# Performance work log

Hardware: AMD Instinct MI355X
Metric: run time of the kernel (lower is better)

## Reference

```python
import jax, jax.numpy as jnp
from jax import lax
import numpy as np


def _gru_layer(x_seq, W_ih, W_hh, b_ih, b_hh):
    """Single GRU layer, torch gate ordering (r, z, n). x_seq: [B, T, I].
    Returns (all hidden states [B, T, H], final hidden [B, H])."""
    B, T, _ = x_seq.shape
    H = W_hh.shape[1]
    # Precompute input projections for all timesteps: [B, T, 3H]
    x_proj = jnp.einsum('bti,gi->btg', x_seq, W_ih) + b_ih

    def step(h, xp):
        hp = h @ W_hh.T + b_hh                       # [B, 3H]
        xr, xz, xn = jnp.split(xp, 3, axis=-1)
        hr, hz, hn = jnp.split(hp, 3, axis=-1)
        r = jax.nn.sigmoid(xr + hr)
        z = jax.nn.sigmoid(xz + hz)
        n = jnp.tanh(xn + r * hn)
        h_new = (1.0 - z) * n + z * h
        return h_new, h_new

    h0 = jnp.zeros((B, H), dtype=x_seq.dtype)
    hT, hs = lax.scan(step, h0, x_proj.transpose(1, 0, 2))  # scan over time
    return hs.transpose(1, 0, 2), hT


def setup_inputs() -> dict:
    key = jax.random.key(0)
    ks = jax.random.split(key, 12)
    B, T, I, H, O = 128, 1000, 64, 512, 1
    s_in = 1.0 / np.sqrt(H)  # torch GRU init scale
    d = {
        'x': jax.random.normal(ks[0], (B, T, I), jnp.float32),
        'W_ih0': jax.random.uniform(ks[1], (3 * H, I), jnp.float32, -s_in, s_in),
        'W_hh0': jax.random.uniform(ks[2], (3 * H, H), jnp.float32, -s_in, s_in),
        'b_ih0': jax.random.uniform(ks[3], (3 * H,), jnp.float32, -s_in, s_in),
        'b_hh0': jax.random.uniform(ks[4], (3 * H,), jnp.float32, -s_in, s_in),
        'W_ih1': jax.random.uniform(ks[5], (3 * H, H), jnp.float32, -s_in, s_in),
        'W_hh1': jax.random.uniform(ks[6], (3 * H, H), jnp.float32, -s_in, s_in),
        'b_ih1': jax.random.uniform(ks[7], (3 * H,), jnp.float32, -s_in, s_in),
        'b_hh1': jax.random.uniform(ks[8], (3 * H,), jnp.float32, -s_in, s_in),
        'W_fc': jax.random.uniform(ks[9], (O, H), jnp.float32, -s_in, s_in),
        'b_fc': jax.random.uniform(ks[10], (O,), jnp.float32, -s_in, s_in),
    }
    return d


def reference(x, W_ih0, W_hh0, b_ih0, b_hh0, W_ih1, W_hh1, b_ih1, b_hh1, W_fc, b_fc):
    # Layer 0 (eval mode: inter-layer dropout is identity)
    h_seq0, _ = _gru_layer(x, W_ih0, W_hh0, b_ih0, b_hh0)
    # Layer 1; final hidden state of the last layer is h_n[-1]
    _, hT1 = _gru_layer(h_seq0, W_ih1, W_hh1, b_ih1, b_hh1)
    out = hT1 @ W_fc.T + b_fc          # [B, O]
    return jax.nn.sigmoid(out)
```

## Files before the change

### kernel.cpp

```cpp
#include <hip/hip_runtime.h>

typedef unsigned int u32;
typedef unsigned short u16;
typedef short bf16x8 __attribute__((ext_vector_type(8)));
typedef float f32x4 __attribute__((ext_vector_type(4)));

#define TLEN 1000
#define BATCH 128
#define IDIM 64
#define HDIM 512

#define NWG 256
#define NTHR 256

#define H0_OFF 0
#define H1_OFF 524288
#define PX0_OFF 1048576
#define PH0_OFF 1245184
#define PX1_OFF 2818048
#define PH1_OFF 4390912
#define FLG_OFF 5963776
#define XSL_OFF 5967872

__device__ __forceinline__ u16 f2bf(float f) {
  u32 u = __float_as_uint(f);
  u += 0x7fffu + ((u >> 16) & 1u);
  return (u16)(u >> 16);
}
__device__ __forceinline__ float bf2f(u16 h) { return __uint_as_float(((u32)h) << 16); }
__device__ __forceinline__ float sigm(float x) { return 1.0f / (1.0f + __expf(-x)); }
__device__ __forceinline__ float tanhfast(float x) {
  float e = __expf(-2.0f * fabsf(x));
  float t = (1.0f - e) / (1.0f + e);
  return x >= 0.0f ? t : -t;
}
__device__ __forceinline__ u32 umin2(u32 a, u32 b) { return a < b ? a : b; }
__device__ __forceinline__ u32 umax2(u32 a, u32 b) { return a > b ? a : b; }

__device__ __forceinline__ void sys_st16(u16* p, u32 v) {
  asm volatile("global_store_short %0, %1, off sc0 sc1" ::"v"(p), "v"(v) : "memory");
}
__device__ __forceinline__ void sys_st32(u32* p, u32 v) {
  asm volatile("global_store_dword %0, %1, off sc0 sc1" ::"v"(p), "v"(v) : "memory");
}
__device__ __forceinline__ uint4 sys_ld128(const u32* p) {
  uint4 v;
  asm volatile("global_load_dwordx4 %0, %1, off sc0 sc1\n\ts_waitcnt vmcnt(0)"
               : "=v"(v) : "v"(p) : "memory");
  return v;
}
__device__ __forceinline__ void sys_ldA(bf16x8& d, const u16* p) {
  asm volatile("global_load_dwordx4 %0, %1, off sc0 sc1" : "=v"(d) : "v"(p));
}
__device__ __forceinline__ void l2_st16(u16* p, u32 v) {
  asm volatile("global_store_short %0, %1, off sc0" ::"v"(p), "v"(v) : "memory");
}
__device__ __forceinline__ void l2_st32(u32* p, u32 v) {
  asm volatile("global_store_dword %0, %1, off sc0" ::"v"(p), "v"(v) : "memory");
}
__device__ __forceinline__ uint4 l2_ld128(const u32* p) {
  uint4 v;
  asm volatile("global_load_dwordx4 %0, %1, off sc0\n\ts_waitcnt vmcnt(0)"
               : "=v"(v) : "v"(p) : "memory");
  return v;
}
__device__ __forceinline__ void l2_ldA(bf16x8& d, const u16* p) {
  asm volatile("global_load_dwordx4 %0, %1, off sc0" : "=v"(d) : "v"(p));
}

__global__ void pack_weights(const float* Wih0, const float* Whh0,
                             const float* Wih1, const float* Whh1, char* ws) {
  int fid = blockIdx.x * NTHR + threadIdx.x;
  const float* src;
  int K, Kks;
  size_t obase;
  int f = fid;
  if (f < 12288) {
    src = Wih0; K = 64; Kks = 2; obase = PX0_OFF;
  } else if (f < 12288 + 98304) {
    f -= 12288; src = Whh0; K = 512; Kks = 16; obase = PH0_OFF;
  } else if (f < 12288 + 2 * 98304) {
    f -= 12288 + 98304; src = Wih1; K = 512; Kks = 16; obase = PX1_OFF;
  } else if (f < 12288 + 3 * 98304) {
    f -= 12288 + 2 * 98304; src = Whh1; K = 512; Kks = 16; obase = PH1_OFF;
  } else {
    return;
  }
  int lane = f & 63;
  int r = f >> 6;
  int ks = r % Kks; r /= Kks;
  int ct = r % 3;
  int sl = r / 3;
  int grow = ct * 512 + sl * 16 + (lane & 15);
  int k = ks * 32 + ((lane >> 4) * 8);
  const float* s = src + (size_t)grow * K + k;
  u32 p0 = f2bf(s[0]) | ((u32)f2bf(s[1]) << 16);
  u32 p1 = f2bf(s[2]) | ((u32)f2bf(s[3]) << 16);
  u32 p2 = f2bf(s[4]) | ((u32)f2bf(s[5]) << 16);
  u32 p3 = f2bf(s[6]) | ((u32)f2bf(s[7]) << 16);
  *(uint4*)(ws + obase + (size_t)f * 16) = make_uint4(p0, p1, p2, p3);
}

struct KP {
  const float *x, *bih0, *bhh0, *bih1, *bhh1, *Wfc, *bfc;
  float* out;
  char* ws;
};

#define MFMA(A, B, C) __builtin_amdgcn_mfma_f32_16x16x32_bf16((A), (B), (C), 0, 0, 0)

__device__ __forceinline__ void wait_flags(const u32* fl0s, const u32* fl1s,
                                           const u32* fl0f, const u32* fl1f,
                                           u32 bias, u32 k) {
  if (threadIdx.x < 64) {
    const int lane = threadIdx.x;
    for (;;) {
      u32 m = 0xFFFFFFFFu;
      if (lane < 4) {
        uint4 v = sys_ld128(fl0s + lane * 4);
        m = umin2(umin2(v.x, v.y), umin2(v.z, v.w));
      } else if (lane < 8) {
        uint4 v = sys_ld128(fl1s + (lane - 4) * 4);
        m = umin2(umin2(v.x, v.y), umin2(v.z, v.w)) + bias;
      } else if (lane < 12) {
        uint4 v = l2_ld128(fl0f + (lane - 8) * 4);
        m = umin2(umin2(v.x, v.y), umin2(v.z, v.w));
      } else if (lane < 16) {
        uint4 v = l2_ld128(fl1f + (lane - 12) * 4);
        m = umin2(umin2(v.x, v.y), umin2(v.z, v.w)) + bias;
      }
      m = umax2(m, __shfl_xor(m, 8));
      m = umin2(m, __shfl_xor(m, 4));
      m = umin2(m, __shfl_xor(m, 2));
      m = umin2(m, __shfl_xor(m, 1));
      if (__shfl(m, 0) >= k) break;
      __builtin_amdgcn_s_sleep(1);
    }
  }
  __syncthreads();
}

__global__ __launch_bounds__(NTHR, 1) void gru_main(KP P) {
  __shared__ f32x4 red[4][8][64];
  const int tid = threadIdx.x;
  const int lane = tid & 63;
  const int w = tid >> 6;
  const int b = blockIdx.x;
  const int bg = b & 7;
  const int q = b >> 3;
  const int layer = q & 1;
  const int colWG = q >> 1;

  char* ws = P.ws;
  u16* h0 = (u16*)(ws + H0_OFF);
  u16* h1 = (u16*)(ws + H1_OFF);
  u32* fb = (u32*)(ws + FLG_OFF) + bg * 128;
  u32* fl0s = fb;
  u32* fl1s = fb + 32;
  u32* fl0f = fb + 64;
  u32* fl1f = fb + 96;
  u32* xsl = (u32*)(ws + XSL_OFF) + bg * 64;
  u32* phf = xsl + 32;
  const bf16x8* px = (const bf16x8*)(ws + (layer ? PX1_OFF : PX0_OFF));
  const bf16x8* ph = (const bf16x8*)(ws + (layer ? PH1_OFF : PH0_OFF));

  u32* mySig_s = (layer ? fl1s : fl0s) + colWG;
  u32* mySig_f = (layer ? fl1f : fl0f) + colWG;

  const float* bih = layer ? P.bih1 : P.bih0;
  const float* bhh = layer ? P.bhh1 : P.bhh0;
  const int cw = w & 1;
  const int jcol = colWG * 32 + cw * 16 + (lane & 15);
  const float b_r = bih[jcol] + bhh[jcol];
  const float b_z = bih[HDIM + jcol] + bhh[HDIM + jcol];
  const float b_nx = bih[2 * HDIM + jcol];
  const float b_nh = bhh[2 * HDIM + jcol];

  const size_t bgoff = (size_t)bg * 16 * HDIM;
  const size_t SLOT = (size_t)BATCH * HDIM;

  bf16x8 xB[3][2][4], hB[3][2][4];
#pragma unroll
  for (int ct = 0; ct < 3; ++ct)
#pragma unroll
    for (int cs = 0; cs < 2; ++cs)
#pragma unroll
      for (int j = 0; j < 4; ++j)
        hB[ct][cs][j] =
            ph[((size_t)((colWG * 2 + cs) * 3 + ct) * 16 + (j * 4 + w)) * 64 + lane];
  if (layer == 0) {
    const bf16x8 z8 = {0, 0, 0, 0, 0, 0, 0, 0};
#pragma unroll
    for (int ct = 0; ct < 3; ++ct)
#pragma unroll
      for (int cs = 0; cs < 2; ++cs)
#pragma unroll
        for (int j = 0; j < 4; ++j) xB[ct][cs][j] = z8;
    if (w < 2) {
#pragma unroll
      for (int ct = 0; ct < 3; ++ct)
#pragma unroll
        for (int cs = 0; cs < 2; ++cs)
          xB[ct][cs][0] = px[((size_t)((colWG * 2 + cs) * 3 + ct) * 2 + w) * 64 + lane];
    }
  } else {
#pragma unroll
    for (int ct = 0; ct < 3; ++ct)
#pragma unroll
      for (int cs = 0; cs < 2; ++cs)
#pragma unroll
        for (int j = 0; j < 4; ++j)
          xB[ct][cs][j] =
              px[((size_t)((colWG * 2 + cs) * 3 + ct) * 16 + (j * 4 + w)) * 64 + lane];
  }

  u32 xcc = 0;
  asm volatile("s_getreg_b32 %0, hwreg(HW_REG_XCC_ID)" : "=s"(xcc));
  if (tid == 0) sys_st32(xsl + q, xcc + 1u);
  __syncthreads();
  if (tid == 0) sys_st32(phf + q, 1u);
  if (tid < 64) {
    for (;;) {
      u32 m = 0xFFFFFFFFu;
      if (lane < 8) {
        uint4 v = sys_ld128(phf + lane * 4);
        m = umin2(umin2(v.x, v.y), umin2(v.z, v.w));
      }
      m = umin2(m, __shfl_xor(m, 1));
      m = umin2(m, __shfl_xor(m, 2));
      m = umin2(m, __shfl_xor(m, 4));
      if (__shfl(m, 0) >= 1u) break;
      __builtin_amdgcn_s_sleep(2);
    }
  }
  __syncthreads();
  u32 mn = 0xFFFFFFFFu, mx = 0u;
  if (lane < 8) {
    uint4 v = sys_ld128(xsl + lane * 4);
    mn = umin2(umin2(v.x, v.y), umin2(v.z, v.w));
    mx = umax2(umax2(v.x, v.y), umax2(v.z, v.w));
  }
  mn = umin2(mn, __shfl_xor(mn, 1)); mx = umax2(mx, __shfl_xor(mx, 1));
  mn = umin2(mn, __shfl_xor(mn, 2)); mx = umax2(mx, __shfl_xor(mx, 2));
  mn = umin2(mn, __shfl_xor(mn, 4)); mx = umax2(mx, __shfl_xor(mx, 4));
  mn = __shfl(mn, 0); mx = __shfl(mx, 0);
  const bool isLocal = (mn != 0u) && (mn == mx);

  const f32x4 zf = {0.f, 0.f, 0.f, 0.f};
  f32x4 hown = zf;

#pragma unroll 1
  for (int k = 0; k <= TLEN; ++k) {
    const bool active = (layer == 0) ? (k < TLEN) : (k >= 1);
    if (active) {
      f32x4 aR[2], aZ[2], aXN[2], aHN[2];
#pragma unroll
      for (int cs = 0; cs < 2; ++cs) { aR[cs] = zf; aZ[cs] = zf; aXN[cs] = zf; aHN[cs] = zf; }
      const u16* h0src = h0 + (size_t)((k + 3) & 3) * SLOT + bgoff;

      if (layer == 0) {
        if (w < 2) {
          const float* s = P.x +
              ((size_t)(bg * 16 + (lane & 15)) * TLEN + k) * IDIM +
              w * 32 + ((lane >> 4) * 8);
          float4 v0 = ((const float4*)s)[0];
          float4 v1 = ((const float4*)s)[1];
          bf16x8 A;
          A[0] = (short)f2bf(v0.x); A[1] = (short)f2bf(v0.y);
          A[2] = (short)f2bf(v0.z); A[3] = (short)f2bf(v0.w);
          A[4] = (short)f2bf(v1.x); A[5] = (short)f2bf(v1.y);
          A[6] = (short)f2bf(v1.z); A[7] = (short)f2bf(v1.w);
#pragma unroll
          for (int cs = 0; cs < 2; ++cs) {
            aR[cs] = MFMA(A, xB[0][cs][0], aR[cs]);
            aZ[cs] = MFMA(A, xB[1][cs][0], aZ[cs]);
            aXN[cs] = MFMA(A, xB[2][cs][0], aXN[cs]);
          }
        }
        if (k > 0) wait_flags(fl0s, fl1s, fl0f, fl1f, 2u, (u32)k);
        bf16x8 A[4];
        if (isLocal) {
#pragma unroll
          for (int j = 0; j < 4; ++j)
            l2_ldA(A[j], h0src + (size_t)(lane & 15) * HDIM + (j * 4 + w) * 32 +
                             ((lane >> 4) * 8));
        } else {
#pragma unroll
          for (int j = 0; j < 4; ++j)
            sys_ldA(A[j], h0src + (size_t)(lane & 15) * HDIM + (j * 4 + w) * 32 +
                              ((lane >> 4) * 8));
        }
        asm volatile("s_waitcnt vmcnt(0)" ::: "memory");
        __builtin_amdgcn_sched_barrier(0);
#pragma unroll
        for (int j = 0; j < 4; ++j)
#pragma unroll
          for (int cs = 0; cs < 2; ++cs) {
            aR[cs] = MFMA(A[j], hB[0][cs][j], aR[cs]);
            aZ[cs] = MFMA(A[j], hB[1][cs][j], aZ[cs]);
            aHN[cs] = MFMA(A[j], hB[2][cs][j], aHN[cs]);
          }
      } else {
        wait_flags(fl0s, fl1s, fl0f, fl1f, 1u, (u32)k);
        const u16* h1src = h1 + (size_t)((k + 2) & 3) * SLOT + bgoff;
        bf16x8 A1[4], A2[4];
        if (isLocal) {
#pragma unroll
          for (int j = 0; j < 4; ++j) {
            const size_t off = (size_t)(lane & 15) * HDIM + (j * 4 + w) * 32 +
                               ((lane >> 4) * 8);
            l2_ldA(A1[j], h0src + off);
            l2_ldA(A2[j], h1src + off);
          }
        } else {
#pragma unroll
          for (int j = 0; j < 4; ++j) {
            const size_t off = (size_t)(lane & 15) * HDIM + (j * 4 + w) * 32 +
                               ((lane >> 4) * 8);
            sys_ldA(A1[j], h0src + off);
            sys_ldA(A2[j], h1src + off);
          }
        }
        asm volatile("s_waitcnt vmcnt(0)" ::: "memory");
        __builtin_amdgcn_sched_barrier(0);
#pragma unroll
        for (int j = 0; j < 4; ++j)
#pragma unroll
          for (int cs = 0; cs < 2; ++cs) {
            aR[cs] = MFMA(A1[j], xB[0][cs][j], aR[cs]);
            aZ[cs] = MFMA(A1[j], xB[1][cs][j], aZ[cs]);
            aXN[cs] = MFMA(A1[j], xB[2][cs][j], aXN[cs]);
          }
#pragma unroll
        for (int j = 0; j < 4; ++j)
#pragma unroll
          for (int cs = 0; cs < 2; ++cs) {
            aR[cs] = MFMA(A2[j], hB[0][cs][j], aR[cs]);
            aZ[cs] = MFMA(A2[j], hB[1][cs][j], aZ[cs]);
            aHN[cs] = MFMA(A2[j], hB[2][cs][j], aHN[cs]);
          }
      }

#pragma unroll
      for (int cs = 0; cs < 2; ++cs) {
        red[w][0 + cs][lane] = aR[cs];
        red[w][2 + cs][lane] = aZ[cs];
        red[w][4 + cs][lane] = aXN[cs];
        red[w][6 + cs][lane] = aHN[cs];
      }
      __syncthreads();
      f32x4 R = zf, Z = zf, XN = zf, HN = zf;
#pragma unroll
      for (int kq = 0; kq < 4; ++kq) {
        R = R + red[kq][0 + cw][lane];
        Z = Z + red[kq][2 + cw][lane];
        XN = XN + red[kq][4 + cw][lane];
        HN = HN + red[kq][6 + cw][lane];
      }
      __syncthreads();

      if (w < 2) {
        u16* hw = (layer ? h1 + (size_t)((k + 3) & 3) * SLOT
                         : h0 + (size_t)(k & 3) * SLOT);
        u32 hv16[4];
        int rowb[4];
#pragma unroll
        for (int qq = 0; qq < 4; ++qq) {
          float r = sigm(R[qq] + b_r);
          float z = sigm(Z[qq] + b_z);
          float n = tanhfast(XN[qq] + b_nx + r * (HN[qq] + b_nh));
          float hv = (1.f - z) * n + z * hown[qq];
          hown[qq] = hv;
          hv16[qq] = (u32)f2bf(hv);
          rowb[qq] = bg * 16 + (lane >> 4) * 4 + qq;
        }
        if (isLocal) {
#pragma unroll
          for (int qq = 0; qq < 4; ++qq)
            l2_st16(&hw[(size_t)rowb[qq] * HDIM + jcol], hv16[qq]);
        } else {
#pragma unroll
          for (int qq = 0; qq < 4; ++qq)
            sys_st16(&hw[(size_t)rowb[qq] * HDIM + jcol], hv16[qq]);
        }
      }

      __syncthreads();
      if (tid == 0) {
        asm volatile("s_waitcnt vmcnt(0)" ::: "memory");
        l2_st32(mySig_f, (u32)(k + 1));
        sys_st32(mySig_s, (u32)(k + 1));
      }
    }
  }

  if (layer == 1 && colWG == 0) {
    if (tid < 64) {
      for (;;) {
        u32 m = 0xFFFFFFFFu;
        if (lane < 4) {
          uint4 v = sys_ld128(fl1s + lane * 4);
          m = umin2(umin2(v.x, v.y), umin2(v.z, v.w));
        } else if (lane < 8) {
          uint4 v = l2_ld128(fl1f + (lane - 4) * 4);
          m = umin2(umin2(v.x, v.y), umin2(v.z, v.w));
        }
        m = umax2(m, __shfl_xor(m, 4));
        m = umin2(m, __shfl_xor(m, 1));
        m = umin2(m, __shfl_xor(m, 2));
        if (__shfl(m, 0) >= (u32)(TLEN + 1)) break;
        __builtin_amdgcn_s_sleep(1);
      }
    }
    __syncthreads();
    const u16* hT = h1 + (size_t)((TLEN + 3) & 3) * SLOT;
    int row = tid >> 4, qq = tid & 15;
    const u16* hr = hT + (size_t)(bg * 16 + row) * HDIM + qq * 32;
    bf16x8 hv[4];
    if (isLocal) {
#pragma unroll
      for (int c = 0; c < 4; ++c) l2_ldA(hv[c], hr + c * 8);
    } else {
#pragma unroll
      for (int c = 0; c < 4; ++c) sys_ldA(hv[c], hr + c * 8);
    }
    asm volatile("s_waitcnt vmcnt(0)" ::: "memory");
    const float* wf = P.Wfc + qq * 32;
    float s = 0.f;
#pragma unroll
    for (int c = 0; c < 4; ++c)
#pragma unroll
      for (int k2 = 0; k2 < 8; ++k2) s += bf2f((u16)hv[c][k2]) * wf[c * 8 + k2];
    s += __shfl_xor(s, 1);
    s += __shfl_xor(s, 2);
    s += __shfl_xor(s, 4);
    s += __shfl_xor(s, 8);
    if (qq == 0) P.out[bg * 16 + row] = sigm(s + P.bfc[0]);
  }
}

extern "C" void kernel_launch(void* const* d_in, const int* in_sizes, int n_in,
                              void* d_out, int out_size, void* d_ws, size_t ws_size,
                              hipStream_t stream) {
  const float* x = (const float*)d_in[0];
  const float* Wih0 = (const float*)d_in[1];
  const float* Whh0 = (const float*)d_in[2];
  const float* bih0 = (const float*)d_in[3];
  const float* bhh0 = (const float*)d_in[4];
  const float* Wih1 = (const float*)d_in[5];
  const float* Whh1 = (const float*)d_in[6];
  const float* bih1 = (const float*)d_in[7];
  const float* bhh1 = (const float*)d_in[8];
  const float* Wfc = (const float*)d_in[9];
  const float* bfc = (const float*)d_in[10];

  hipMemsetAsync(d_ws, 0, 1048576, stream);
  hipMemsetAsync((char*)d_ws + FLG_OFF, 0, 6144, stream);
  pack_weights<<<dim3(1200), dim3(NTHR), 0, stream>>>(Wih0, Whh0, Wih1, Whh1, (char*)d_ws);

  KP P = {x, bih0, bhh0, bih1, bhh1, Wfc, bfc, (float*)d_out, (char*)d_ws};
  void* args[] = {&P};
  hipError_t ce = hipLaunchCooperativeKernel((void*)gru_main, dim3(NWG), dim3(NTHR), args, 0,
                                             stream);
  if (ce != hipSuccess) {
    (void)hipGetLastError();
    gru_main<<<dim3(NWG), dim3(NTHR), 0, stream>>>(P);
  }
}
```

Before: 3.876 ms.

## Fuse both GRU layers into each workgroup, halving the grid to 128

Each workgroup now computes both layers for its column slice instead of assigning layer 0 and layer 1 to separate workgroups. Layer 1 at step k reuses the h0 tile already loaded for layer 0, and a single flag set replaces the two per-layer flag sets. This cuts the number of participants in the cross-workgroup barrier and the redundant h0 loads. In exchange each workgroup runs both layers' MFMA and reduction work serially and holds three weight fragment sets in registers, which raises register pressure and per-step latency.

Result: slower. 4.914 ms (+26.8%).

```diff
diff --git a/kernel.cpp b/kernel.cpp
--- a/kernel.cpp
+++ b/kernel.cpp
@@ -10,7 +10,7 @@
 #define IDIM 64
 #define HDIM 512
 
-#define NWG 256
+#define NWG 128
 #define NTHR 256
 
 #define H0_OFF 0
@@ -109,30 +109,21 @@
 
 #define MFMA(A, B, C) __builtin_amdgcn_mfma_f32_16x16x32_bf16((A), (B), (C), 0, 0, 0)
 
-__device__ __forceinline__ void wait_flags(const u32* fl0s, const u32* fl1s,
-                                           const u32* fl0f, const u32* fl1f,
-                                           u32 bias, u32 k) {
+__device__ __forceinline__ void wait_flags(const u32* fls, const u32* flf, u32 k) {
   if (threadIdx.x < 64) {
     const int lane = threadIdx.x;
     for (;;) {
       u32 m = 0xFFFFFFFFu;
       if (lane < 4) {
-        uint4 v = sys_ld128(fl0s + lane * 4);
+        uint4 v = sys_ld128(fls + lane * 4);
         m = umin2(umin2(v.x, v.y), umin2(v.z, v.w));
       } else if (lane < 8) {
-        uint4 v = sys_ld128(fl1s + (lane - 4) * 4);
-        m = umin2(umin2(v.x, v.y), umin2(v.z, v.w)) + bias;
-      } else if (lane < 12) {
-        uint4 v = l2_ld128(fl0f + (lane - 8) * 4);
+        uint4 v = l2_ld128(flf + (lane - 4) * 4);
         m = umin2(umin2(v.x, v.y), umin2(v.z, v.w));
-      } else if (lane < 16) {
-        uint4 v = l2_ld128(fl1f + (lane - 12) * 4);
-        m = umin2(umin2(v.x, v.y), umin2(v.z, v.w)) + bias;
-      }
-      m = umax2(m, __shfl_xor(m, 8));
-      m = umin2(m, __shfl_xor(m, 4));
+      }
+      m = umax2(m, __shfl_xor(m, 4));
+      m = umin2(m, __shfl_xor(m, 1));
       m = umin2(m, __shfl_xor(m, 2));
-      m = umin2(m, __shfl_xor(m, 1));
       if (__shfl(m, 0) >= k) break;
       __builtin_amdgcn_s_sleep(1);
     }
@@ -147,200 +138,143 @@
   const int w = tid >> 6;
   const int b = blockIdx.x;
   const int bg = b & 7;
-  const int q = b >> 3;
-  const int layer = q & 1;
-  const int colWG = q >> 1;
+  const int colWG = b >> 3;
 
   char* ws = P.ws;
   u16* h0 = (u16*)(ws + H0_OFF);
   u16* h1 = (u16*)(ws + H1_OFF);
   u32* fb = (u32*)(ws + FLG_OFF) + bg * 128;
-  u32* fl0s = fb;
-  u32* fl1s = fb + 32;
-  u32* fl0f = fb + 64;
-  u32* fl1f = fb + 96;
+  u32* fls = fb;
+  u32* flf = fb + 32;
   u32* xsl = (u32*)(ws + XSL_OFF) + bg * 64;
   u32* phf = xsl + 32;
-  const bf16x8* px = (const bf16x8*)(ws + (layer ? PX1_OFF : PX0_OFF));
-  const bf16x8* ph = (const bf16x8*)(ws + (layer ? PH1_OFF : PH0_OFF));
-
-  u32* mySig_s = (layer ? fl1s : fl0s) + colWG;
-  u32* mySig_f = (layer ? fl1f : fl0f) + colWG;
-
-  const float* bih = layer ? P.bih1 : P.bih0;
-  const float* bhh = layer ? P.bhh1 : P.bhh0;
+  const bf16x8* px0 = (const bf16x8*)(ws + PX0_OFF);
+  const bf16x8* ph0 = (const bf16x8*)(ws + PH0_OFF);
+  const bf16x8* px1 = (const bf16x8*)(ws + PX1_OFF);
+  const bf16x8* ph1 = (const bf16x8*)(ws + PH1_OFF);
+
   const int cw = w & 1;
   const int jcol = colWG * 32 + cw * 16 + (lane & 15);
-  const float b_r = bih[jcol] + bhh[jcol];
-  const float b_z = bih[HDIM + jcol] + bhh[HDIM + jcol];
-  const float b_nx = bih[2 * HDIM + jcol];
-  const float b_nh = bhh[2 * HDIM + jcol];
+  const float b_r0 = P.bih0[jcol] + P.bhh0[jcol];
+  const float b_z0 = P.bih0[HDIM + jcol] + P.bhh0[HDIM + jcol];
+  const float b_nx0 = P.bih0[2 * HDIM + jcol];
+  const float b_nh0 = P.bhh0[2 * HDIM + jcol];
+  const float b_r1 = P.bih1[jcol] + P.bhh1[jcol];
+  const float b_z1 = P.bih1[HDIM + jcol] + P.bhh1[HDIM + jcol];
+  const float b_nx1 = P.bih1[2 * HDIM + jcol];
+  const float b_nh1 = P.bhh1[2 * HDIM + jcol];
 
   const size_t bgoff = (size_t)bg * 16 * HDIM;
   const size_t SLOT = (size_t)BATCH * HDIM;
 
-  bf16x8 xB[3][2][4], hB[3][2][4];
+  bf16x8 xB0[3][2];
+  bf16x8 hB0[3][2][4], xB1[3][2][4], hB1[3][2][4];
 #pragma unroll
   for (int ct = 0; ct < 3; ++ct)
 #pragma unroll
-    for (int cs = 0; cs < 2; ++cs)
-#pragma unroll
-      for (int j = 0; j < 4; ++j)
-        hB[ct][cs][j] =
-            ph[((size_t)((colWG * 2 + cs) * 3 + ct) * 16 + (j * 4 + w)) * 64 + lane];
-  if (layer == 0) {
-    const bf16x8 z8 = {0, 0, 0, 0, 0, 0, 0, 0};
-#pragma unroll
-    for (int ct = 0; ct < 3; ++ct)
-#pragma unroll
-      for (int cs = 0; cs < 2; ++cs)
-#pragma unroll
-        for (int j = 0; j < 4; ++j) xB[ct][cs][j] = z8;
-    if (w < 2) {
-#pragma unroll
-      for (int ct = 0; ct < 3; ++ct)
-#pragma unroll
-        for (int cs = 0; cs < 2; ++cs)
-          xB[ct][cs][0] = px[((size_t)((colWG * 2 + cs) * 3 + ct) * 2 + w) * 64 + lane];
-    }
-  } else {
-#pragma unroll
-    for (int ct = 0; ct < 3; ++ct)
-#pragma unroll
-      for (int cs = 0; cs < 2; ++cs)
-#pragma unroll
-        for (int j = 0; j < 4; ++j)
-          xB[ct][cs][j] =
-              px[((size_t)((colWG * 2 + cs) * 3 + ct) * 16 + (j * 4 + w)) * 64 + lane];
-  }
+    for (int cs = 0; cs < 2; ++cs) {
+      const int sl = colWG * 2 + cs;
+#pragma unroll
+      for (int j = 0; j < 4; ++j) {
+        hB0[ct][cs][j] = ph0[((size_t)(sl * 3 + ct) * 16 + (j * 4 + w)) * 64 + lane];
+        xB1[ct][cs][j] = px1[((size_t)(sl * 3 + ct) * 16 + (j * 4 + w)) * 64 + lane];
+        hB1[ct][cs][j] = ph1[((size_t)(sl * 3 + ct) * 16 + (j * 4 + w)) * 64 + lane];
+      }
+      if (w < 2) xB0[ct][cs] = px0[((size_t)(sl * 3 + ct) * 2 + w) * 64 + lane];
+      else { const bf16x8 z8 = {0,0,0,0,0,0,0,0}; xB0[ct][cs] = z8; }
+    }
 
   u32 xcc = 0;
   asm volatile("s_getreg_b32 %0, hwreg(HW_REG_XCC_ID)" : "=s"(xcc));
-  if (tid == 0) sys_st32(xsl + q, xcc + 1u);
+  if (tid == 0) sys_st32(xsl + colWG, xcc + 1u);
   __syncthreads();
-  if (tid == 0) sys_st32(phf + q, 1u);
+  if (tid == 0) sys_st32(phf + colWG, 1u);
   if (tid < 64) {
     for (;;) {
       u32 m = 0xFFFFFFFFu;
-      if (lane < 8) {
+      if (lane < 4) {
         uint4 v = sys_ld128(phf + lane * 4);
         m = umin2(umin2(v.x, v.y), umin2(v.z, v.w));
       }
       m = umin2(m, __shfl_xor(m, 1));
       m = umin2(m, __shfl_xor(m, 2));
-      m = umin2(m, __shfl_xor(m, 4));
       if (__shfl(m, 0) >= 1u) break;
       __builtin_amdgcn_s_sleep(2);
     }
   }
   __syncthreads();
   u32 mn = 0xFFFFFFFFu, mx = 0u;
-  if (lane < 8) {
+  if (lane < 4) {
     uint4 v = sys_ld128(xsl + lane * 4);
     mn = umin2(umin2(v.x, v.y), umin2(v.z, v.w));
     mx = umax2(umax2(v.x, v.y), umax2(v.z, v.w));
   }
   mn = umin2(mn, __shfl_xor(mn, 1)); mx = umax2(mx, __shfl_xor(mx, 1));
   mn = umin2(mn, __shfl_xor(mn, 2)); mx = umax2(mx, __shfl_xor(mx, 2));
-  mn = umin2(mn, __shfl_xor(mn, 4)); mx = umax2(mx, __shfl_xor(mx, 4));
   mn = __shfl(mn, 0); mx = __shfl(mx, 0);
   const bool isLocal = (mn != 0u) && (mn == mx);
 
   const f32x4 zf = {0.f, 0.f, 0.f, 0.f};
-  f32x4 hown = zf;
+  f32x4 hown0 = zf, hown1 = zf;
 
 #pragma unroll 1
   for (int k = 0; k <= TLEN; ++k) {
-    const bool active = (layer == 0) ? (k < TLEN) : (k >= 1);
-    if (active) {
-      f32x4 aR[2], aZ[2], aXN[2], aHN[2];
-#pragma unroll
-      for (int cs = 0; cs < 2; ++cs) { aR[cs] = zf; aZ[cs] = zf; aXN[cs] = zf; aHN[cs] = zf; }
-      const u16* h0src = h0 + (size_t)((k + 3) & 3) * SLOT + bgoff;
-
-      if (layer == 0) {
-        if (w < 2) {
-          const float* s = P.x +
-              ((size_t)(bg * 16 + (lane & 15)) * TLEN + k) * IDIM +
-              w * 32 + ((lane >> 4) * 8);
-          float4 v0 = ((const float4*)s)[0];
-          float4 v1 = ((const float4*)s)[1];
-          bf16x8 A;
-          A[0] = (short)f2bf(v0.x); A[1] = (short)f2bf(v0.y);
-          A[2] = (short)f2bf(v0.z); A[3] = (short)f2bf(v0.w);
-          A[4] = (short)f2bf(v1.x); A[5] = (short)f2bf(v1.y);
-          A[6] = (short)f2bf(v1.z); A[7] = (short)f2bf(v1.w);
-#pragma unroll
-          for (int cs = 0; cs < 2; ++cs) {
-            aR[cs] = MFMA(A, xB[0][cs][0], aR[cs]);
-            aZ[cs] = MFMA(A, xB[1][cs][0], aZ[cs]);
-            aXN[cs] = MFMA(A, xB[2][cs][0], aXN[cs]);
-          }
+    const bool doL0 = (k < TLEN);
+    const bool doL1 = (k >= 1);
+    f32x4 aR[2], aZ[2], aXN[2], aHN[2];
+#pragma unroll
+    for (int cs = 0; cs < 2; ++cs) { aR[cs] = zf; aZ[cs] = zf; aXN[cs] = zf; aHN[cs] = zf; }
+
+    if (doL0 && w < 2) {
+      const float* s = P.x + ((size_t)(bg * 16 + (lane & 15)) * TLEN + k) * IDIM +
+                       w * 32 + ((lane >> 4) * 8);
+      float4 v0 = ((const float4*)s)[0];
+      float4 v1 = ((const float4*)s)[1];
+      bf16x8 A;
+      A[0] = (short)f2bf(v0.x); A[1] = (short)f2bf(v0.y);
+      A[2] = (short)f2bf(v0.z); A[3] = (short)f2bf(v0.w);
+      A[4] = (short)f2bf(v1.x); A[5] = (short)f2bf(v1.y);
+      A[6] = (short)f2bf(v1.z); A[7] = (short)f2bf(v1.w);
+#pragma unroll
+      for (int cs = 0; cs < 2; ++cs) {
+        aR[cs] = MFMA(A, xB0[0][cs], aR[cs]);
+        aZ[cs] = MFMA(A, xB0[1][cs], aZ[cs]);
+        aXN[cs] = MFMA(A, xB0[2][cs], aXN[cs]);
+      }
+    }
+
+    if (k > 0) wait_flags(fls, flf, (u32)k);
+
+    const u16* h0src = h0 + (size_t)((k + 3) & 3) * SLOT + bgoff;
+    const u16* h1src = h1 + (size_t)((k + 2) & 3) * SLOT + bgoff;
+    bf16x8 A0[4], A1[4];
+    if (isLocal) {
+#pragma unroll
+      for (int j = 0; j < 4; ++j) {
+        const size_t off = (size_t)(lane & 15) * HDIM + (j * 4 + w) * 32 + ((lane >> 4) * 8);
+        l2_ldA(A0[j], h0src + off);
+        if (doL1) l2_ldA(A1[j], h1src + off);
+      }
+    } else {
+#pragma unroll
+      for (int j = 0; j < 4; ++j) {
+        const size_t off = (size_t)(lane & 15) * HDIM + (j * 4 + w) * 32 + ((lane >> 4) * 8);
+        sys_ldA(A0[j], h0src + off);
+        if (doL1) sys_ldA(A1[j], h1src + off);
+      }
+    }
+    asm volatile("s_waitcnt vmcnt(0)" ::: "memory");
+    __builtin_amdgcn_sched_barrier(0);
+
+    if (doL0) {
+#pragma unroll
+      for (int j = 0; j < 4; ++j)
+#pragma unroll
+        for (int cs = 0; cs < 2; ++cs) {
+          aR[cs] = MFMA(A0[j], hB0[0][cs][j], aR[cs]);
+          aZ[cs] = MFMA(A0[j], hB0[1][cs][j], aZ[cs]);
+          aHN[cs] = MFMA(A0[j], hB0[2][cs][j], aHN[cs]);
         }
-        if (k > 0) wait_flags(fl0s, fl1s, fl0f, fl1f, 2u, (u32)k);
-        bf16x8 A[4];
-        if (isLocal) {
-#pragma unroll
-          for (int j = 0; j < 4; ++j)
-            l2_ldA(A[j], h0src + (size_t)(lane & 15) * HDIM + (j * 4 + w) * 32 +
-                             ((lane >> 4) * 8));
-        } else {
-#pragma unroll
-          for (int j = 0; j < 4; ++j)
-            sys_ldA(A[j], h0src + (size_t)(lane & 15) * HDIM + (j * 4 + w) * 32 +
-                              ((lane >> 4) * 8));
-        }
-        asm volatile("s_waitcnt vmcnt(0)" ::: "memory");
-        __builtin_amdgcn_sched_barrier(0);
-#pragma unroll
-        for (int j = 0; j < 4; ++j)
-#pragma unroll
-          for (int cs = 0; cs < 2; ++cs) {
-            aR[cs] = MFMA(A[j], hB[0][cs][j], aR[cs]);
-            aZ[cs] = MFMA(A[j], hB[1][cs][j], aZ[cs]);
-            aHN[cs] = MFMA(A[j], hB[2][cs][j], aHN[cs]);
-          }
-      } else {
-        wait_flags(fl0s, fl1s, fl0f, fl1f, 1u, (u32)k);
-        const u16* h1src = h1 + (size_t)((k + 2) & 3) * SLOT + bgoff;
-        bf16x8 A1[4], A2[4];
-        if (isLocal) {
-#pragma unroll
-          for (int j = 0; j < 4; ++j) {
-            const size_t off = (size_t)(lane & 15) * HDIM + (j * 4 + w) * 32 +
-                               ((lane >> 4) * 8);
-            l2_ldA(A1[j], h0src + off);
-            l2_ldA(A2[j], h1src + off);
-          }
-        } else {
-#pragma unroll
-          for (int j = 0; j < 4; ++j) {
-            const size_t off = (size_t)(lane & 15) * HDIM + (j * 4 + w) * 32 +
-                               ((lane >> 4) * 8);
-            sys_ldA(A1[j], h0src + off);
-            sys_ldA(A2[j], h1src + off);
-          }
-        }
-        asm volatile("s_waitcnt vmcnt(0)" ::: "memory");
-        __builtin_amdgcn_sched_barrier(0);
-#pragma unroll
-        for (int j = 0; j < 4; ++j)
-#pragma unroll
-          for (int cs = 0; cs < 2; ++cs) {
-            aR[cs] = MFMA(A1[j], xB[0][cs][j], aR[cs]);
-            aZ[cs] = MFMA(A1[j], xB[1][cs][j], aZ[cs]);
-            aXN[cs] = MFMA(A1[j], xB[2][cs][j], aXN[cs]);
-          }
-#pragma unroll
-        for (int j = 0; j < 4; ++j)
-#pragma unroll
-          for (int cs = 0; cs < 2; ++cs) {
-            aR[cs] = MFMA(A2[j], hB[0][cs][j], aR[cs]);
-            aZ[cs] = MFMA(A2[j], hB[1][cs][j], aZ[cs]);
-            aHN[cs] = MFMA(A2[j], hB[2][cs][j], aHN[cs]);
-          }
-      }
-
 #pragma unroll
       for (int cs = 0; cs < 2; ++cs) {
         red[w][0 + cs][lane] = aR[cs];
@@ -358,61 +292,84 @@
         HN = HN + red[kq][6 + cw][lane];
       }
       __syncthreads();
-
       if (w < 2) {
-        u16* hw = (layer ? h1 + (size_t)((k + 3) & 3) * SLOT
-                         : h0 + (size_t)(k & 3) * SLOT);
-        u32 hv16[4];
-        int rowb[4];
+        u16* hw = h0 + (size_t)(k & 3) * SLOT;
 #pragma unroll
         for (int qq = 0; qq < 4; ++qq) {
-          float r = sigm(R[qq] + b_r);
-          float z = sigm(Z[qq] + b_z);
-          float n = tanhfast(XN[qq] + b_nx + r * (HN[qq] + b_nh));
-          float hv = (1.f - z) * n + z * hown[qq];
-          hown[qq] = hv;
-          hv16[qq] = (u32)f2bf(hv);
-          rowb[qq] = bg * 16 + (lane >> 4) * 4 + qq;
+          float r = sigm(R[qq] + b_r0);
+          float z = sigm(Z[qq] + b_z0);
+          float n = tanhfast(XN[qq] + b_nx0 + r * (HN[qq] + b_nh0));
+          float hv = (1.f - z) * n + z * hown0[qq];
+          hown0[qq] = hv;
+          int rowb = bg * 16 + (lane >> 4) * 4 + qq;
+          if (isLocal) l2_st16(&hw[(size_t)rowb * HDIM + jcol], (u32)f2bf(hv));
+          else sys_st16(&hw[(size_t)rowb * HDIM + jcol], (u32)f2bf(hv));
         }
-        if (isLocal) {
-#pragma unroll
-          for (int qq = 0; qq < 4; ++qq)
-            l2_st16(&hw[(size_t)rowb[qq] * HDIM + jcol], hv16[qq]);
-        } else {
-#pragma unroll
-          for (int qq = 0; qq < 4; ++qq)
-            sys_st16(&hw[(size_t)rowb[qq] * HDIM + jcol], hv16[qq]);
+      }
+    }
+
+    if (doL1) {
+#pragma unroll
+      for (int cs = 0; cs < 2; ++cs) { aR[cs] = zf; aZ[cs] = zf; aXN[cs] = zf; aHN[cs] = zf; }
+#pragma unroll
+      for (int j = 0; j < 4; ++j)
+#pragma unroll
+        for (int cs = 0; cs < 2; ++cs) {
+          aR[cs] = MFMA(A0[j], xB1[0][cs][j], aR[cs]);
+          aZ[cs] = MFMA(A0[j], xB1[1][cs][j], aZ[cs]);
+          aXN[cs] = MFMA(A0[j], xB1[2][cs][j], aXN[cs]);
         }
-      }
-
+#pragma unroll
+      for (int j = 0; j < 4; ++j)
+#pragma unroll
+        for (int cs = 0; cs < 2; ++cs) {
+          aR[cs] = MFMA(A1[j], hB1[0][cs][j], aR[cs]);
+          aZ[cs] = MFMA(A1[j], hB1[1][cs][j], aZ[cs]);
+          aHN[cs] = MFMA(A1[j], hB1[2][cs][j], aHN[cs]);
+        }
+#pragma unroll
+      for (int cs = 0; cs < 2; ++cs) {
+        red[w][0 + cs][lane] = aR[cs];
+        red[w][2 + cs][lane] = aZ[cs];
+        red[w][4 + cs][lane] = aXN[cs];
+        red[w][6 + cs][lane] = aHN[cs];
+      }
       __syncthreads();
-      if (tid == 0) {
-        asm volatile("s_waitcnt vmcnt(0)" ::: "memory");
-        l2_st32(mySig_f, (u32)(k + 1));
-        sys_st32(mySig_s, (u32)(k + 1));
-      }
-    }
-  }
-
-  if (layer == 1 && colWG == 0) {
-    if (tid < 64) {
-      for (;;) {
-        u32 m = 0xFFFFFFFFu;
-        if (lane < 4) {
-          uint4 v = sys_ld128(fl1s + lane * 4);
-          m = umin2(umin2(v.x, v.y), umin2(v.z, v.w));
-        } else if (lane < 8) {
-          uint4 v = l2_ld128(fl1f + (lane - 4) * 4);
-          m = umin2(umin2(v.x, v.y), umin2(v.z, v.w));
+      f32x4 R = zf, Z = zf, XN = zf, HN = zf;
+#pragma unroll
+      for (int kq = 0; kq < 4; ++kq) {
+        R = R + red[kq][0 + cw][lane];
+        Z = Z + red[kq][2 + cw][lane];
+        XN = XN + red[kq][4 + cw][lane];
+        HN = HN + red[kq][6 + cw][lane];
+      }
+      __syncthreads();
+      if (w < 2) {
+        u16* hw = h1 + (size_t)((k + 3) & 3) * SLOT;
+#pragma unroll
+        for (int qq = 0; qq < 4; ++qq) {
+          float r = sigm(R[qq] + b_r1);
+          float z = sigm(Z[qq] + b_z1);
+          float n = tanhfast(XN[qq] + b_nx1 + r * (HN[qq] + b_nh1));
+          float hv = (1.f - z) * n + z * hown1[qq];
+          hown1[qq] = hv;
+          int rowb = bg * 16 + (lane >> 4) * 4 + qq;
+          if (isLocal) l2_st16(&hw[(size_t)rowb * HDIM + jcol], (u32)f2bf(hv));
+          else sys_st16(&hw[(size_t)rowb * HDIM + jcol], (u32)f2bf(hv));
         }
-        m = umax2(m, __shfl_xor(m, 4));
-        m = umin2(m, __shfl_xor(m, 1));
-        m = umin2(m, __shfl_xor(m, 2));
-        if (__shfl(m, 0) >= (u32)(TLEN + 1)) break;
-        __builtin_amdgcn_s_sleep(1);
-      }
-    }
+      }
+    }
+
     __syncthreads();
+    if (tid == 0) {
+      asm volatile("s_waitcnt vmcnt(0)" ::: "memory");
+      l2_st32(flf + colWG, (u32)(k + 1));
+      sys_st32(fls + colWG, (u32)(k + 1));
+    }
+  }
+
+  if (colWG == 0) {
+    wait_flags(fls, flf, (u32)(TLEN + 1));
     const u16* hT = h1 + (size_t)((TLEN + 3) & 3) * SLOT;
     int row = tid >> 4, qq = tid & 15;
     const u16* hr = hT + (size_t)(bg * 16 + row) * HDIM + qq * 32;
```
